# Kernel tuning notes

Hardware: AMD Instinct MI355X
Metric: run time of the kernel (lower is better)

The kernel has to match this reference:

```python
import jax, jax.numpy as jnp
import numpy as np

D_MODEL = 512
NUM_HEADS = 8
HEAD_DIM = 64  # D_MODEL // NUM_HEADS


def setup_inputs() -> dict:
    key = jax.random.key(0)
    kq, kk, kv, kw, kb = jax.random.split(key, 5)
    B, S = 2, 2048
    query = jax.random.normal(kq, (B, S, D_MODEL), dtype=jnp.float32)
    key_t = jax.random.normal(kk, (B, S, D_MODEL), dtype=jnp.float32)
    value = jax.random.normal(kv, (B, S, D_MODEL), dtype=jnp.float32)
    # shared projection (nn.Linear(d_models, d_models)) applied to q, k, v
    scale = 1.0 / np.sqrt(D_MODEL)
    W = jax.random.uniform(kw, (D_MODEL, D_MODEL), dtype=jnp.float32, minval=-scale, maxval=scale)
    b = jax.random.uniform(kb, (D_MODEL,), dtype=jnp.float32, minval=-scale, maxval=scale)
    return {"query": query, "key": key_t, "value": value, "W": W, "b": b}


def reference(query, key, value, W, b):
    B, S, _ = query.shape
    H, Dh = NUM_HEADS, HEAD_DIM

    def proj(x):  # nn.Linear + ReLU, shared across q/k/v
        return jax.nn.relu(jnp.einsum('bsd,ed->bse', x, W) + b)

    # [B, S, d] -> [B, H, S, Dh]
    split = lambda x: proj(x).reshape(B, S, H, Dh).transpose(0, 2, 1, 3)
    Q, K, V = split(query), split(key), split(value)

    scores = jnp.einsum('bhqd,bhkd->bhqk', Q, K) / jnp.sqrt(jnp.float32(Dh))
    causal_mask = jnp.triu(jnp.ones((S, S), dtype=bool), k=1)  # True above diagonal
    scores = jnp.where(causal_mask, -jnp.inf, scores)
    attn = jax.nn.softmax(scores, axis=-1)
    out = jnp.einsum('bhqk,bhkd->bhqd', attn, V)  # [B, H, S, Dh]

    # faithful to original: transpose(0,1) swaps batch and heads, then view
    final = jnp.swapaxes(out, 0, 1).reshape(B, -1, D_MODEL)  # [B, S, d_model]
    return final
```

## Files before the change

### kernel.cpp

```cpp
#include <hip/hip_runtime.h>
#include <hip/hip_bf16.h>
#include <cstdint>
#include <cstddef>

typedef __bf16 bf16_t;
typedef bf16_t bf16x8 __attribute__((ext_vector_type(8)));
typedef float f32x4 __attribute__((ext_vector_type(4)));
typedef float f32x16 __attribute__((ext_vector_type(16)));
typedef unsigned short u16;
typedef u16 u16x8 __attribute__((ext_vector_type(8)));

#define S_LEN 2048
#define NB 2
#define NH 8
#define DHD 64
#define DM 512

static __device__ __forceinline__ u16 bfbits(float f) {
  union { __bf16 h; u16 u; } c; c.h = (__bf16)f; return c.u;
}
static __device__ __forceinline__ float bits2f(u16 b) {
  union { u16 u; __bf16 h; } c; c.u = b; return (float)c.h;
}
static __device__ __forceinline__ uint32_t pkbf(float a, float b) {
  union { __bf16 h[2]; uint32_t u; } c;
  c.h[0] = (__bf16)a; c.h[1] = (__bf16)b;
  return c.u;
}
static __device__ __forceinline__ void gload16(const void* g, void* l) {
  __builtin_amdgcn_global_load_lds(
      (const __attribute__((address_space(1))) uint32_t*)g,
      (__attribute__((address_space(3))) uint32_t*)l, 16, 0, 0);
}

static __device__ __forceinline__ int slot_of(int bh, int t32, int chunk) {
  int qb = t32 >> 2;
  int nc = (2 * (qb + 1) + 9) / 10;
  int off;
  if (qb < 10) off = (qb - 5) * 8;
  else if (qb < 15) off = 40 + (qb - 10) * 12;
  else off = 100;
  return bh * 116 + off + (t32 & 3) * nc + chunk;
}

__launch_bounds__(256, 2)
__global__ void proj_kernel(const float* __restrict__ Xq, const float* __restrict__ Xk,
                            const float* __restrict__ Xv, const float* __restrict__ W,
                            const float* __restrict__ bias,
                            u16* __restrict__ Qw, u16* __restrict__ Kw,
                            u16* __restrict__ Vt64) {
  __shared__ __align__(16) float BUF[2][8192];
  const int bid = blockIdx.x;
  const int xcd = bid & 7;
  const int u = bid >> 3;
  const int n0 = (u & 3) * 128;
  const int mIdx = u >> 2;
  const int mg = (xcd * 12 + mIdx) * 128;
  const int z = mg >> 12;
  const int m_in = mg & 4095;
  const int b = m_in >> 11;
  const int s0m = m_in & (S_LEN - 1);
  const int h0 = n0 >> 6;
  const float* __restrict__ X = (z == 0) ? Xq : ((z == 1) ? Xk : Xv);
  X += (size_t)m_in * DM;

  const int t = threadIdx.x;
  const int lane = t & 63;
  const int wid = t >> 6;
  const int wr = wid >> 1, wc = wid & 1;
  const int fr = lane & 15, fg = lane >> 4;

  f32x4 acc[4][4] = {};

  const int lrow = lane >> 3;
  const int lblk = lane & 7;

  auto stage = [&](int bf, int k0) {
    #pragma unroll
    for (int i = 0; i < 4; ++i) {
      int c = wid * 4 + i;
      int r = c * 8 + lrow;
      gload16(X + (size_t)r * DM + k0 + ((lblk ^ (r & 7)) << 2), &BUF[bf][c * 256]);
    }
    #pragma unroll
    for (int i = 0; i < 4; ++i) {
      int c = wid * 4 + i;
      int r = c * 8 + lrow;
      gload16(W + (size_t)(n0 + r) * DM + k0 + ((lblk ^ (r & 7)) << 2),
              &BUF[bf][4096 + c * 256]);
    }
  };

  stage(0, 0);
  int cb = 0;
  for (int i = 0; i < 16; ++i) {
    __syncthreads();
    if (i < 15) stage(cb ^ 1, (i + 1) * 32);
    const float* Ac = BUF[cb];
    bf16x8 af[4], bfr[4];
    #pragma unroll
    for (int m2 = 0; m2 < 4; ++m2) {
      int r = wr*64 + m2*16 + fr;
      f32x4 lo = *(const f32x4*)&Ac[r*32 + (((2*fg)     ^ (r & 7)) << 2)];
      f32x4 hi = *(const f32x4*)&Ac[r*32 + (((2*fg + 1) ^ (r & 7)) << 2)];
      union { u16x8 s; bf16x8 v; } f;
      f.s[0]=bfbits(lo[0]); f.s[1]=bfbits(lo[1]); f.s[2]=bfbits(lo[2]); f.s[3]=bfbits(lo[3]);
      f.s[4]=bfbits(hi[0]); f.s[5]=bfbits(hi[1]); f.s[6]=bfbits(hi[2]); f.s[7]=bfbits(hi[3]);
      af[m2] = f.v;
    }
    #pragma unroll
    for (int ni = 0; ni < 4; ++ni) {
      int r = wc*64 + ni*16 + fr;
      f32x4 lo = *(const f32x4*)&Ac[4096 + r*32 + (((2*fg)     ^ (r & 7)) << 2)];
      f32x4 hi = *(const f32x4*)&Ac[4096 + r*32 + (((2*fg + 1) ^ (r & 7)) << 2)];
      union { u16x8 s; bf16x8 v; } f;
      f.s[0]=bfbits(lo[0]); f.s[1]=bfbits(lo[1]); f.s[2]=bfbits(lo[2]); f.s[3]=bfbits(lo[3]);
      f.s[4]=bfbits(hi[0]); f.s[5]=bfbits(hi[1]); f.s[6]=bfbits(hi[2]); f.s[7]=bfbits(hi[3]);
      bfr[ni] = f.v;
    }
    __builtin_amdgcn_s_setprio(1);
    #pragma unroll
    for (int m2 = 0; m2 < 4; ++m2)
      #pragma unroll
      for (int ni = 0; ni < 4; ++ni)
        acc[m2][ni] = __builtin_amdgcn_mfma_f32_16x16x32_bf16(af[m2], bfr[ni], acc[m2][ni], 0, 0, 0);
    __builtin_amdgcn_s_setprio(0);
    cb ^= 1;
  }
  __syncthreads();

  const float QSCALE = 0.125f * 1.44269504089f;
  u16* epi = (u16*)&BUF[0][0];

  if (z == 2) {
    #pragma unroll
    for (int m2 = 0; m2 < 4; ++m2) {
      #pragma unroll
      for (int ni = 0; ni < 4; ++ni) {
        int e = wc*64 + ni*16 + fr;
        int m = wr*64 + m2*16 + fg*4;
        float bv = bias[n0 + e];
        float v0 = fmaxf(acc[m2][ni][0] + bv, 0.f);
        float v1 = fmaxf(acc[m2][ni][1] + bv, 0.f);
        float v2 = fmaxf(acc[m2][ni][2] + bv, 0.f);
        float v3 = fmaxf(acc[m2][ni][3] + bv, 0.f);
        uint2 w; w.x = pkbf(v0, v1); w.y = pkbf(v2, v3);
        *(uint2*)&epi[e*136 + m] = w;
      }
    }
    __syncthreads();
    const int e2 = t >> 1, mc = (t & 1) * 64;
    const int h = h0 + (e2 >> 6), d = e2 & 63;
    const int sb = (s0m >> 6) + (mc >> 6);
    u16* dst = Vt64 + (((size_t)(b * NH + h) * 32 + sb) * 64 + d) * 64;
    #pragma unroll
    for (int i = 0; i < 8; ++i)
      *(uint4*)(dst + i*8) = *(const uint4*)&epi[e2*136 + mc + i*8];
  } else {
    #pragma unroll
    for (int m2 = 0; m2 < 4; ++m2) {
      #pragma unroll
      for (int ni = 0; ni < 4; ++ni) {
        int e = wc*64 + ni*16 + fr;
        float bv = bias[n0 + e];
        #pragma unroll
        for (int r = 0; r < 4; ++r) {
          float v = acc[m2][ni][r] + bv;
          if (z == 0) v *= QSCALE;
          v = fmaxf(v, 0.f);
          epi[(wr*64 + m2*16 + fg*4 + r)*136 + e] = bfbits(v);
        }
      }
    }
    __syncthreads();
    const int mrow = t >> 1, hf = t & 1;
    u16* dst = ((z == 0) ? Qw : Kw) +
               (((size_t)(b * NH + h0 + hf)) * S_LEN + s0m + mrow) * DHD;
    #pragma unroll
    for (int i = 0; i < 8; ++i)
      *(uint4*)(dst + i*8) = *(const uint4*)&epi[mrow*136 + hf*64 + i*8];
  }
}

static __device__ const uint8_t QBT[34] = {4,5,6,7,8,9,9,10,10,11,11,12,12,13,13,14,14,14,15,15,15,
                                           3,8,13, 2,7,12, 1,6,11, 0,5,10,15};
static __device__ const uint8_t CKT[34] = {0,0,0,0,0,0,1,0,1,0,1,0,1,0,1,0,1,2,0,1,2,
                                           0,1,2, 0,1,2, 0,1,2, 0,1,2,3};

__launch_bounds__(256, 2)
__global__ void attn_kernel(const u16* __restrict__ Qw, const u16* __restrict__ Kw,
                            const u16* __restrict__ Vt64, u16* __restrict__ Opart,
                            float* __restrict__ lbuf, float* __restrict__ out) {
  __shared__ u16 KLDS[4][4096];
  __shared__ u16 VLDS[4][4096];
  const int t = threadIdx.x;
  const int lane = t & 63;
  const int wid = t >> 6;
  const int lam = lane & 31;
  const int hi = lane >> 5;
  const int h8 = hi << 3, h4 = hi << 2;
  const int bid = blockIdx.x;
  const int bh = bid & 15;
  const int u = bid >> 4;
  const int qb = QBT[u], chunk = CKT[u];
  const int steps_total = (qb + 1) * 2;
  const int sc0 = chunk * 10;
  const int sc1e = sc0 + 10;
  const int sc1 = (sc1e < steps_total) ? sc1e : steps_total;
  const int t32 = qb * 4 + wid;
  const int q0 = qb * 128 + wid * 32;

  const u16* __restrict__ Qh = Qw + (size_t)bh * S_LEN * DHD;
  const u16* __restrict__ Kh = Kw + (size_t)bh * S_LEN * DHD;
  const u16* __restrict__ V64 = Vt64 + (size_t)bh * 32 * 64 * 64;

  bf16x8 qf[4];
  #pragma unroll
  for (int c = 0; c < 4; ++c)
    qf[c] = *(const bf16x8*)(Qh + (size_t)(q0 + lam) * DHD + c*16 + h8);

  const int lrow = lane >> 3;
  const int lblk = lane & 7;
  auto stage = [&](int bf, int s) {
    #pragma unroll
    for (int i = 0; i < 2; ++i) {
      int c = wid * 2 + i;
      int r = c * 8 + lrow;
      int sw = (lblk ^ (r & 7)) << 3;
      gload16(Kh + (size_t)(s * 64 + r) * 64 + sw, &KLDS[bf][c * 512]);
      gload16(V64 + ((size_t)s * 64 + r) * 64 + sw, &VLDS[bf][c * 512]);
    }
  };

  f32x16 o0 = {}, o1 = {};
  float lsum = 0.f;

  auto softpack = [&](const f32x16& sc, bool msk, bf16x8& pb0v, bf16x8& pb1v) {
    float p[16];
    #pragma unroll
    for (int r = 0; r < 16; ++r) {
      float ev = __builtin_amdgcn_exp2f(sc[r]);
      int kc = (r & 3) + ((r >> 2) << 3) + h4;
      if (msk && kc > lam) ev = 0.f;
      p[r] = ev;
      lsum += ev;
    }
    uint32_t X0 = pkbf(p[0], p[1]),  X1 = pkbf(p[2], p[3]);
    uint32_t X2 = pkbf(p[4], p[5]),  X3 = pkbf(p[6], p[7]);
    uint32_t X4 = pkbf(p[8], p[9]),  X5 = pkbf(p[10], p[11]);
    uint32_t X6 = pkbf(p[12], p[13]), X7 = pkbf(p[14], p[15]);
    asm("v_permlane32_swap_b32 %0, %1" : "+v"(X0), "+v"(X2));
    asm("v_permlane32_swap_b32 %0, %1" : "+v"(X1), "+v"(X3));
    asm("v_permlane32_swap_b32 %0, %1" : "+v"(X4), "+v"(X6));
    asm("v_permlane32_swap_b32 %0, %1" : "+v"(X5), "+v"(X7));
    union U8 { uint32_t u[4]; bf16x8 v; };
    U8 a, bU;
    a.u[0] = X0; a.u[1] = X1; a.u[2] = X2; a.u[3] = X3;
    bU.u[0] = X4; bU.u[1] = X5; bU.u[2] = X6; bU.u[3] = X7;
    pb0v = a.v; pb1v = bU.v;
  };

  auto do_step = [&](int s, int buf) {
    const int d2 = t32 - 2 * s;
    bf16x8 a0, a1, b0v, b1v;
    f32x16 sA = {}, sB = {};
    if (d2 >= 0) {
      bf16x8 kA[4];
      #pragma unroll
      for (int c = 0; c < 4; ++c) {
        int r = lam, e = ((2*c + hi) ^ (r & 7)) * 8;
        kA[c] = *(const bf16x8*)&KLDS[buf][r*64 + e];
      }
      __builtin_amdgcn_s_setprio(1);
      #pragma unroll
      for (int c = 0; c < 4; ++c)
        sA = __builtin_amdgcn_mfma_f32_32x32x16_bf16(kA[c], qf[c], sA, 0, 0, 0);
      __builtin_amdgcn_s_setprio(0);
    }
    if (d2 >= 1) {
      bf16x8 kB[4];
      #pragma unroll
      for (int c = 0; c < 4; ++c) {
        int r = 32 + lam, e = ((2*c + hi) ^ (r & 7)) * 8;
        kB[c] = *(const bf16x8*)&KLDS[buf][r*64 + e];
      }
      __builtin_amdgcn_s_setprio(1);
      #pragma unroll
      for (int c = 0; c < 4; ++c)
        sB = __builtin_amdgcn_mfma_f32_32x32x16_bf16(kB[c], qf[c], sB, 0, 0, 0);
      __builtin_amdgcn_s_setprio(0);
    }
    if (d2 >= 0) softpack(sA, d2 == 0, a0, a1);
    if (d2 >= 1) softpack(sB, d2 == 1, b0v, b1v);
    if (d2 >= 0) {
      bf16x8 v0[2], v1[2];
      #pragma unroll
      for (int c2 = 0; c2 < 2; ++c2) {
        int r0 = lam,      e0 = ((2*c2 + hi) ^ (r0 & 7)) * 8;
        int r1 = 32 + lam, e1 = ((2*c2 + hi) ^ (r1 & 7)) * 8;
        v0[c2] = *(const bf16x8*)&VLDS[buf][r0*64 + e0];
        v1[c2] = *(const bf16x8*)&VLDS[buf][r1*64 + e1];
      }
      __builtin_amdgcn_s_setprio(1);
      o0 = __builtin_amdgcn_mfma_f32_32x32x16_bf16(v0[0], a0, o0, 0, 0, 0);
      o0 = __builtin_amdgcn_mfma_f32_32x32x16_bf16(v0[1], a1, o0, 0, 0, 0);
      o1 = __builtin_amdgcn_mfma_f32_32x32x16_bf16(v1[0], a0, o1, 0, 0, 0);
      o1 = __builtin_amdgcn_mfma_f32_32x32x16_bf16(v1[1], a1, o1, 0, 0, 0);
      __builtin_amdgcn_s_setprio(0);
    }
    if (d2 >= 1) {
      bf16x8 v0[2], v1[2];
      #pragma unroll
      for (int c2 = 0; c2 < 2; ++c2) {
        int r0 = lam,      e0 = ((4 + 2*c2 + hi) ^ (r0 & 7)) * 8;
        int r1 = 32 + lam, e1 = ((4 + 2*c2 + hi) ^ (r1 & 7)) * 8;
        v0[c2] = *(const bf16x8*)&VLDS[buf][r0*64 + e0];
        v1[c2] = *(const bf16x8*)&VLDS[buf][r1*64 + e1];
      }
      __builtin_amdgcn_s_setprio(1);
      o0 = __builtin_amdgcn_mfma_f32_32x32x16_bf16(v0[0], b0v, o0, 0, 0, 0);
      o0 = __builtin_amdgcn_mfma_f32_32x32x16_bf16(v0[1], b1v, o0, 0, 0, 0);
      o1 = __builtin_amdgcn_mfma_f32_32x32x16_bf16(v1[0], b0v, o1, 0, 0, 0);
      o1 = __builtin_amdgcn_mfma_f32_32x32x16_bf16(v1[1], b1v, o1, 0, 0, 0);
      __builtin_amdgcn_s_setprio(0);
    }
  };

  stage(0, sc0);
  stage(1, sc0 + 1);
  int ib = 0;
  for (int s = sc0; s < sc1; s += 2) {
    __syncthreads();
    if (s + 2 < sc1) {
      stage((ib + 2) & 3, s + 2);
      stage((ib + 3) & 3, s + 3);
    }
    do_step(s, ib);
    do_step(s + 1, (ib + 1) & 3);
    ib = (ib + 2) & 3;
  }

  float l = lsum + __shfl_xor(lsum, 32);

  if (qb <= 4) {
    const int b = bh >> 3, hh = bh & 7;
    const float inv = 1.0f / l;
    float* orow = out + (((size_t)(hh * NB + b)) * S_LEN + (q0 + lam)) * DHD;
    #pragma unroll
    for (int r = 0; r < 16; ++r) {
      int d = (r & 3) + ((r >> 2) << 3) + h4;
      orow[d] = o0[r] * inv;
      orow[d + 32] = o1[r] * inv;
    }
  } else {
    const int slot = slot_of(bh, t32, chunk);
    uint32_t w[16] __attribute__((aligned(16)));
    #pragma unroll
    for (int m = 0; m < 8; ++m) {
      w[m]     = pkbf(o0[2*m], o0[2*m+1]);
      w[8 + m] = pkbf(o1[2*m], o1[2*m+1]);
    }
    u16* op = Opart + (size_t)slot * 2048 + (size_t)lane * 32;
    #pragma unroll
    for (int i = 0; i < 4; ++i)
      *(uint4*)(op + i*8) = *(const uint4*)&w[i*4];
    if (lane < 32) lbuf[slot * 32 + lane] = l;
  }
}

__launch_bounds__(256)
__global__ void reduce_kernel(const u16* __restrict__ Opart,
                              const float* __restrict__ lbuf,
                              float* __restrict__ out) {
  const int t = threadIdx.x;
  const int unit = blockIdx.x * 4 + (t >> 6);
  const int bh = unit & 15;
  const int ti = 20 + (unit >> 4);
  const int qb = ti >> 2;
  const int nc = (2 * (qb + 1) + 9) / 10;
  const int lane = t & 63;
  const int lam = lane & 31;
  const int h4 = (lane >> 5) << 2;
  const int slot0 = slot_of(bh, ti, 0);

  float O[32];
  #pragma unroll
  for (int i = 0; i < 32; ++i) O[i] = 0.f;
  float L = 0.f;

  for (int c = 0; c < nc; ++c) {
    const u16* op = Opart + (size_t)(slot0 + c) * 2048 + (size_t)lane * 32;
    L += lbuf[(slot0 + c) * 32 + lam];
    #pragma unroll
    for (int i = 0; i < 4; ++i) {
      uint4 v = *(const uint4*)(op + i*8);
      uint32_t a[4] = {v.x, v.y, v.z, v.w};
      #pragma unroll
      for (int jj = 0; jj < 4; ++jj) {
        O[i*8 + 2*jj]     += bits2f((u16)(a[jj] & 0xFFFFu));
        O[i*8 + 2*jj + 1] += bits2f((u16)(a[jj] >> 16));
      }
    }
  }

  const int b = bh >> 3, hh = bh & 7;
  const float inv = 1.0f / L;
  float* orow = out + (((size_t)(hh * NB + b)) * S_LEN + (ti*32 + lam)) * DHD;
  #pragma unroll
  for (int r = 0; r < 16; ++r) {
    int d = (r & 3) + ((r >> 2) << 3) + h4;
    orow[d] = O[r] * inv;
    orow[d + 32] = O[16 + r] * inv;
  }
}

extern "C" void kernel_launch(void* const* d_in, const int* in_sizes, int n_in,
                              void* d_out, int out_size, void* d_ws, size_t ws_size,
                              hipStream_t stream) {
  const float* q = (const float*)d_in[0];
  const float* k = (const float*)d_in[1];
  const float* v = (const float*)d_in[2];
  const float* W = (const float*)d_in[3];
  const float* b = (const float*)d_in[4];

  const size_t elems = (size_t)NB * NH * S_LEN * DHD;
  u16* Qw = (u16*)d_ws;
  u16* Kw = Qw + elems;
  u16* Vt64 = Kw + elems;
  u16* Opart = Vt64 + elems;
  float* lbuf = (float*)(Opart + (size_t)1856 * 2048);

  proj_kernel<<<dim3(384), dim3(256), 0, stream>>>(q, k, v, W, b, Qw, Kw, Vt64);

  attn_kernel<<<dim3(544), dim3(256), 0, stream>>>(Qw, Kw, Vt64, Opart, lbuf, (float*)d_out);

  reduce_kernel<<<dim3(176), dim3(256), 0, stream>>>(Opart, lbuf, (float*)d_out);
}
```

Before: 49.35 us.

## Pre-convert inputs and weights to bf16 and use a 4-stage bf16 projection pipeline

Adds a separate conversion kernel that casts q, k, v and W from fp32 to bf16 in workspace. The projection GEMM then streams bf16 tiles, which halves its global and LDS traffic and removes the per-step fp32-to-bf16 conversion in the inner loop. Staging becomes four buffers with two k-steps in flight per barrier. The cost is an extra kernel launch plus a full read and write of the inputs, and Opart now aliases the bf16 staging area.

```diff
diff --git a/kernel.cpp b/kernel.cpp
--- a/kernel.cpp
+++ b/kernel.cpp
@@ -43,13 +43,29 @@
   return bh * 116 + off + (t32 & 3) * nc + chunk;
 }
 
+__launch_bounds__(256)
+__global__ void cvt_kernel(const float* __restrict__ q, const float* __restrict__ k,
+                           const float* __restrict__ v, const float* __restrict__ W,
+                           u16* __restrict__ dst) {
+  const int z = blockIdx.y;
+  if (z == 3 && blockIdx.x >= 128) return;
+  const float* __restrict__ src = (z == 0) ? q : (z == 1) ? k : (z == 2) ? v : W;
+  u16* __restrict__ d = dst + (size_t)z * 2097152;
+  size_t i = ((size_t)blockIdx.x * 256 + threadIdx.x) * 8;
+  float4 a = *reinterpret_cast<const float4*>(src + i);
+  float4 b = *reinterpret_cast<const float4*>(src + i + 4);
+  u16x8 r;
+  r[0] = bfbits(a.x); r[1] = bfbits(a.y); r[2] = bfbits(a.z); r[3] = bfbits(a.w);
+  r[4] = bfbits(b.x); r[5] = bfbits(b.y); r[6] = bfbits(b.z); r[7] = bfbits(b.w);
+  *reinterpret_cast<u16x8*>(d + i) = r;
+}
+
 __launch_bounds__(256, 2)
-__global__ void proj_kernel(const float* __restrict__ Xq, const float* __restrict__ Xk,
-                            const float* __restrict__ Xv, const float* __restrict__ W,
+__global__ void proj_kernel(const u16* __restrict__ Xall, const u16* __restrict__ Wb,
                             const float* __restrict__ bias,
                             u16* __restrict__ Qw, u16* __restrict__ Kw,
                             u16* __restrict__ Vt64) {
-  __shared__ __align__(16) float BUF[2][8192];
+  __shared__ __align__(16) u16 BUF[4][8192];
   const int bid = blockIdx.x;
   const int xcd = bid & 7;
   const int u = bid >> 3;
@@ -61,8 +77,7 @@
   const int b = m_in >> 11;
   const int s0m = m_in & (S_LEN - 1);
   const int h0 = n0 >> 6;
-  const float* __restrict__ X = (z == 0) ? Xq : ((z == 1) ? Xk : Xv);
-  X += (size_t)m_in * DM;
+  const u16* __restrict__ X = Xall + (size_t)z * 2097152 + (size_t)m_in * DM;
 
   const int t = threadIdx.x;
   const int lane = t & 63;
@@ -72,51 +87,37 @@
 
   f32x4 acc[4][4] = {};
 
-  const int lrow = lane >> 3;
-  const int lblk = lane & 7;
+  const int lrow = lane >> 2;
+  const int lblk = lane & 3;
 
   auto stage = [&](int bf, int k0) {
     #pragma unroll
-    for (int i = 0; i < 4; ++i) {
-      int c = wid * 4 + i;
-      int r = c * 8 + lrow;
-      gload16(X + (size_t)r * DM + k0 + ((lblk ^ (r & 7)) << 2), &BUF[bf][c * 256]);
-    }
-    #pragma unroll
-    for (int i = 0; i < 4; ++i) {
-      int c = wid * 4 + i;
-      int r = c * 8 + lrow;
-      gload16(W + (size_t)(n0 + r) * DM + k0 + ((lblk ^ (r & 7)) << 2),
-              &BUF[bf][4096 + c * 256]);
+    for (int i = 0; i < 2; ++i) {
+      int c = wid * 2 + i;
+      int r = c * 16 + lrow;
+      gload16(X + (size_t)r * DM + k0 + ((lblk ^ (r & 3)) << 3), &BUF[bf][c * 512]);
+    }
+    #pragma unroll
+    for (int i = 0; i < 2; ++i) {
+      int c = wid * 2 + i;
+      int r = c * 16 + lrow;
+      gload16(Wb + (size_t)(n0 + r) * DM + k0 + ((lblk ^ (r & 3)) << 3),
+              &BUF[bf][4096 + c * 512]);
     }
   };
 
-  stage(0, 0);
-  int cb = 0;
-  for (int i = 0; i < 16; ++i) {
-    __syncthreads();
-    if (i < 15) stage(cb ^ 1, (i + 1) * 32);
-    const float* Ac = BUF[cb];
+  auto do_step = [&](int buf) {
+    const u16* Bc = &BUF[buf][0];
     bf16x8 af[4], bfr[4];
     #pragma unroll
     for (int m2 = 0; m2 < 4; ++m2) {
       int r = wr*64 + m2*16 + fr;
-      f32x4 lo = *(const f32x4*)&Ac[r*32 + (((2*fg)     ^ (r & 7)) << 2)];
-      f32x4 hi = *(const f32x4*)&Ac[r*32 + (((2*fg + 1) ^ (r & 7)) << 2)];
-      union { u16x8 s; bf16x8 v; } f;
-      f.s[0]=bfbits(lo[0]); f.s[1]=bfbits(lo[1]); f.s[2]=bfbits(lo[2]); f.s[3]=bfbits(lo[3]);
-      f.s[4]=bfbits(hi[0]); f.s[5]=bfbits(hi[1]); f.s[6]=bfbits(hi[2]); f.s[7]=bfbits(hi[3]);
-      af[m2] = f.v;
+      af[m2] = *(const bf16x8*)&Bc[r*32 + ((fg ^ (r & 3)) << 3)];
     }
     #pragma unroll
     for (int ni = 0; ni < 4; ++ni) {
       int r = wc*64 + ni*16 + fr;
-      f32x4 lo = *(const f32x4*)&Ac[4096 + r*32 + (((2*fg)     ^ (r & 7)) << 2)];
-      f32x4 hi = *(const f32x4*)&Ac[4096 + r*32 + (((2*fg + 1) ^ (r & 7)) << 2)];
-      union { u16x8 s; bf16x8 v; } f;
-      f.s[0]=bfbits(lo[0]); f.s[1]=bfbits(lo[1]); f.s[2]=bfbits(lo[2]); f.s[3]=bfbits(lo[3]);
-      f.s[4]=bfbits(hi[0]); f.s[5]=bfbits(hi[1]); f.s[6]=bfbits(hi[2]); f.s[7]=bfbits(hi[3]);
-      bfr[ni] = f.v;
+      bfr[ni] = *(const bf16x8*)&Bc[4096 + r*32 + ((fg ^ (r & 3)) << 3)];
     }
     __builtin_amdgcn_s_setprio(1);
     #pragma unroll
@@ -125,12 +126,25 @@
       for (int ni = 0; ni < 4; ++ni)
         acc[m2][ni] = __builtin_amdgcn_mfma_f32_16x16x32_bf16(af[m2], bfr[ni], acc[m2][ni], 0, 0, 0);
     __builtin_amdgcn_s_setprio(0);
-    cb ^= 1;
+  };
+
+  stage(0, 0);
+  stage(1, 32);
+  int ib = 0;
+  for (int i = 0; i < 16; i += 2) {
+    __syncthreads();
+    if (i + 2 < 16) {
+      stage((ib + 2) & 3, (i + 2) * 32);
+      stage((ib + 3) & 3, (i + 3) * 32);
+    }
+    do_step(ib);
+    do_step((ib + 1) & 3);
+    ib = (ib + 2) & 3;
   }
   __syncthreads();
 
   const float QSCALE = 0.125f * 1.44269504089f;
-  u16* epi = (u16*)&BUF[0][0];
+  u16* epi = &BUF[0][0];
 
   if (z == 2) {
     #pragma unroll
@@ -427,10 +441,14 @@
   u16* Qw = (u16*)d_ws;
   u16* Kw = Qw + elems;
   u16* Vt64 = Kw + elems;
-  u16* Opart = Vt64 + elems;
-  float* lbuf = (float*)(Opart + (size_t)1856 * 2048);
-
-  proj_kernel<<<dim3(384), dim3(256), 0, stream>>>(q, k, v, W, b, Qw, Kw, Vt64);
+  u16* Xb = Vt64 + elems;
+  u16* Wb = Xb + 3 * elems;
+  u16* Opart = Xb;
+  float* lbuf = (float*)(Wb + 262144);
+
+  cvt_kernel<<<dim3(1024, 4), dim3(256), 0, stream>>>(q, k, v, W, Xb);
+
+  proj_kernel<<<dim3(384), dim3(256), 0, stream>>>(Xb, Wb, b, Qw, Kw, Vt64);
 
   attn_kernel<<<dim3(544), dim3(256), 0, stream>>>(Qw, Kw, Vt64, Opart, lbuf, (float*)d_out);
 
```

New measurement: 56.28 us. 14.0% more time.
